# Kernel optimization log

Measured on AMD Instinct MI355X. Metric: run time of the kernel, lower is better.

The kernel has to match this reference:

```python
import jax, jax.numpy as jnp
import numpy as np
import math

DIM = 1536; NH = 12; HD = 128
F, H, W = 6, 30, 30
S = F * H * W
B = 1
K_LEN = 9900  # hardcoded k_lens in the source forward
EPS_NORM = 1e-6


def _rope_tables(max_len=1024, d=HD):
    # Wan rope_params: three tables of widths d-4*(d//6), 2*(d//6), 2*(d//6)
    # -> cos/sin tables of half-widths 22, 21, 21 (concat = d//2 = 64)
    def ang(dd):
        inv = 1.0 / (10000.0 ** (np.arange(0, dd, 2, dtype=np.float64) / dd))
        return np.outer(np.arange(max_len, dtype=np.float64), inv)
    a = np.concatenate([ang(d - 4 * (d // 6)), ang(2 * (d // 6)), ang(2 * (d // 6))], axis=1)
    return np.cos(a).astype(np.float32), np.sin(a).astype(np.float32)


def setup_inputs() -> dict:
    key = jax.random.key(0)
    ks = jax.random.split(key, 5)
    s = 1.0 / math.sqrt(DIM)
    cos, sin = _rope_tables()
    return {
        "x": jax.random.normal(ks[0], (B, S, DIM), jnp.float32),
        "q_w": jax.random.normal(ks[1], (DIM, DIM), jnp.float32) * s,
        "q_b": jnp.zeros((DIM,), jnp.float32),
        "k_w": jax.random.normal(ks[2], (DIM, DIM), jnp.float32) * s,
        "k_b": jnp.zeros((DIM,), jnp.float32),
        "v_w": jax.random.normal(ks[3], (DIM, DIM), jnp.float32) * s,
        "v_b": jnp.zeros((DIM,), jnp.float32),
        "o_w": jax.random.normal(ks[4], (DIM, DIM), jnp.float32) * s,
        "o_b": jnp.zeros((DIM,), jnp.float32),
        "norm_q_w": jnp.ones((DIM,), jnp.float32),
        "norm_k_w": jnp.ones((DIM,), jnp.float32),
        "freqs_cos": jnp.asarray(cos),
        "freqs_sin": jnp.asarray(sin),
        "grid_f": F, "grid_h": H, "grid_w": W,
    }


def rms_norm(x, w):
    # RMSNorm over full model dim, computed in fp32 (as in source)
    xf = x.astype(jnp.float32)
    xn = xf * jax.lax.rsqrt(jnp.mean(xf * xf, axis=-1, keepdims=True) + EPS_NORM)
    return xn.astype(x.dtype) * w


def rope_apply(x, cos, sin, f, h, w):
    # x: [B,S,N,D]; rotate consecutive pairs with 3D-factorized (f,h,w) freqs
    Bb, Ss, Nn, Dd = x.shape
    c = Dd // 2
    sp = [c - 2 * (c // 3), c // 3, c // 3]  # 22, 21, 21

    def grid(tab):
        tf = tab[:, :sp[0]]
        th = tab[:, sp[0]:sp[0] + sp[1]]
        tw = tab[:, sp[0] + sp[1]:]
        g = jnp.concatenate([
            jnp.broadcast_to(tf[:f, None, None, :], (f, h, w, sp[0])),
            jnp.broadcast_to(th[None, :h, None, :], (f, h, w, sp[1])),
            jnp.broadcast_to(tw[None, None, :w, :], (f, h, w, sp[2])),
        ], axis=-1)
        return g.reshape(f * h * w, 1, c)  # [S,1,c] (broadcast over heads)

    gc, gs = grid(cos), grid(sin)
    xp = x.astype(jnp.float32).reshape(Bb, Ss, Nn, c, 2)
    xr, xi = xp[..., 0], xp[..., 1]
    orr = xr * gc - xi * gs
    oii = xr * gs + xi * gc
    return jnp.stack([orr, oii], axis=-1).reshape(Bb, Ss, Nn, Dd).astype(x.dtype)


def attention(q, k, v, k_len):
    # full attention (window_size=(-1,-1)) with keys masked beyond k_len
    scale = 1.0 / math.sqrt(q.shape[-1])
    att = jnp.einsum('bqnd,bknd->bnqk', q, k) * scale
    valid = jnp.arange(k.shape[1]) < k_len
    att = jnp.where(valid[None, None, None, :], att, jnp.finfo(att.dtype).min)
    p = jax.nn.softmax(att, axis=-1)
    return jnp.einsum('bnqk,bknd->bqnd', p, v)


def reference(x, q_w, q_b, k_w, k_b, v_w, v_b, o_w, o_b, norm_q_w, norm_k_w, freqs_cos, freqs_sin, grid_f, grid_h, grid_w):
    Bb, Ss, _ = x.shape
    q = rms_norm(x @ q_w.T + q_b, norm_q_w).reshape(Bb, Ss, NH, HD)
    k = rms_norm(x @ k_w.T + k_b, norm_k_w).reshape(Bb, Ss, NH, HD)
    v = (x @ v_w.T + v_b).reshape(Bb, Ss, NH, HD)
    q = rope_apply(q, freqs_cos, freqs_sin, grid_f, grid_h, grid_w)
    k = rope_apply(k, freqs_cos, freqs_sin, grid_f, grid_h, grid_w)
    o = attention(q, k, v, K_LEN).reshape(Bb, Ss, NH * HD)
    return o @ o_w.T + o_b
```

## Files before the change

kernel.cpp:

```cpp
#include <hip/hip_runtime.h>

#define DIM 1536
#define NH 12
#define HD 128
#define S_LEN 5400
#define SPAD 5440
#define MPAD 5504
#define MPAD2 5632
#define NQKV 4608
#define EPS_NORM 1e-6f

typedef __bf16 bf16_t;
typedef __bf16 bf16x8 __attribute__((ext_vector_type(8)));
typedef __bf16 bf16x4 __attribute__((ext_vector_type(4)));
typedef __bf16 bf16x2 __attribute__((ext_vector_type(2)));
typedef float  f32x4  __attribute__((ext_vector_type(4)));
typedef float  f32x16 __attribute__((ext_vector_type(16)));
typedef int    i32x2  __attribute__((ext_vector_type(2)));

#define GLOAD_LDS16(gp, lp) __builtin_amdgcn_global_load_lds( \
    (__attribute__((address_space(1))) void*)(void*)(gp),     \
    (__attribute__((address_space(3))) void*)(lp), 16, 0, 0)

__device__ __forceinline__ unsigned int pkbf(float a, float b) {
  union { bf16x2 h; unsigned int u; } c;
  c.h[0] = (__bf16)a; c.h[1] = (__bf16)b;
  return c.u;
}

__device__ __forceinline__ float xhalf_max(float x) {
  i32x2 r = __builtin_amdgcn_permlane32_swap(__float_as_int(x), __float_as_int(x),
                                             false, false);
  return fmaxf(__int_as_float(r.x), __int_as_float(r.y));
}
__device__ __forceinline__ float xhalf_sum(float x) {
  i32x2 r = __builtin_amdgcn_permlane32_swap(__float_as_int(x), __float_as_int(x),
                                             false, false);
  return __int_as_float(r.x) + __int_as_float(r.y);
}


#define CVT_NX 8448
#define CVT_NW 6912
#define CVT_NO 2304

__global__ __launch_bounds__(256) void cvt_all_kernel(
    const float* __restrict__ x, const float* __restrict__ qw,
    const float* __restrict__ kw, const float* __restrict__ vw,
    const float* __restrict__ ow, bf16_t* __restrict__ xb,
    bf16_t* __restrict__ wqkv, bf16_t* __restrict__ wob) {
  int b = blockIdx.x;
  if (b < CVT_NX) {
    size_t base = ((size_t)b * 256 + threadIdx.x) * 4;
    size_t row = base / DIM;
    float4 v = make_float4(0.f, 0.f, 0.f, 0.f);
    if (row < S_LEN) v = *(const float4*)&x[base];
    bf16x4 o; o[0] = (__bf16)v.x; o[1] = (__bf16)v.y; o[2] = (__bf16)v.z; o[3] = (__bf16)v.w;
    *(bf16x4*)&xb[base] = o;
  } else if (b < CVT_NX + CVT_NW) {
    size_t base = ((size_t)(b - CVT_NX) * 256 + threadIdx.x) * 4;
    int row = (int)(base / DIM);
    int col = (int)(base - (size_t)row * DIM);
    const float* src; int rr = row;
    if (rr >= 3072)      { src = vw; rr -= 3072; }
    else if (rr >= 1536) { src = kw; rr -= 1536; }
    else                 { src = qw; }
    float4 v = *(const float4*)&src[(size_t)rr * DIM + col];
    bf16x4 o; o[0] = (__bf16)v.x; o[1] = (__bf16)v.y; o[2] = (__bf16)v.z; o[3] = (__bf16)v.w;
    *(bf16x4*)&wqkv[base] = o;
  } else {
    size_t base = ((size_t)(b - CVT_NX - CVT_NW) * 256 + threadIdx.x) * 4;
    float4 v = *(const float4*)&ow[base];
    bf16x4 o; o[0] = (__bf16)v.x; o[1] = (__bf16)v.y; o[2] = (__bf16)v.z; o[3] = (__bf16)v.w;
    *(bf16x4*)&wob[base] = o;
  }
}


__global__ __launch_bounds__(512, 2) void gemm1_256_kernel(
    const bf16_t* __restrict__ A, const bf16_t* __restrict__ B,
    bf16_t* __restrict__ C, bf16_t* __restrict__ vt,
    const float* __restrict__ bias0, const float* __restrict__ bias1,
    const float* __restrict__ bias2) {
  const int K = 1536, N = NQKV, KT = 24;
  __shared__ bf16_t lds[2][2][256 * 64];
  int tid = threadIdx.x;
  int lane = tid & 63, wave = tid >> 6, quad = lane >> 4, l16 = lane & 15;
  int wm2 = wave >> 2, wn4 = wave & 3;
  int m0 = blockIdx.y * 256, n0 = blockIdx.x * 256;
  const bf16_t* Ab = A + (size_t)m0 * K;
  const bf16_t* Bb = B + (size_t)n0 * K;
  f32x4 acc[8][4] = {};

  int srow = tid >> 3, spc = tid & 7;
  int ldst = srow * 64 + spc * 8;
  int sc8 = (spc ^ (srow & 7)) * 8;

#define G1_STAGE(buf, op, q, kt) \
  GLOAD_LDS16((op ? Bb : Ab) + (size_t)((q) * 64 + srow) * K + (kt) + sc8, \
              &lds[buf][op][(q) * 64 * 64 + ldst])

  G1_STAGE(0, 1, 0, 0); G1_STAGE(0, 1, 1, 0);
  G1_STAGE(0, 1, 2, 0); G1_STAGE(0, 1, 3, 0);
  G1_STAGE(0, 0, 0, 0); G1_STAGE(0, 0, 2, 0);
  G1_STAGE(0, 0, 1, 0); G1_STAGE(0, 0, 3, 0);

  int pcq0 = (0 * 4 + quad) ^ (l16 & 7);
  int pcq1 = (1 * 4 + quad) ^ (l16 & 7);

  for (int t = 0; t < KT; t++) {
    int cur = t & 1, nxt = cur ^ 1;
    int kn = (t + 1) * 64;
    bool st = (t + 1 < KT);

#define G1_PHASE(mh, nh2, STAGES, WAITS)                                      \
    {                                                                         \
      WAITS;                                                                  \
      __builtin_amdgcn_s_barrier();                                           \
      __builtin_amdgcn_sched_barrier(0);                                      \
      bf16x8 af[4][2], bfv[2][2];                                             \
      _Pragma("unroll")                                                       \
      for (int i2 = 0; i2 < 4; i2++) {                                        \
        int row = wm2 * 128 + ((mh) * 4 + i2) * 16 + l16;                     \
        af[i2][0] = *(const bf16x8*)&lds[cur][0][row * 64 + pcq0 * 8];        \
        af[i2][1] = *(const bf16x8*)&lds[cur][0][row * 64 + pcq1 * 8];        \
      }                                                                       \
      _Pragma("unroll")                                                       \
      for (int j2 = 0; j2 < 2; j2++) {                                        \
        int rowb = wn4 * 64 + ((nh2) * 2 + j2) * 16 + l16;                    \
        bfv[j2][0] = *(const bf16x8*)&lds[cur][1][rowb * 64 + pcq0 * 8];      \
        bfv[j2][1] = *(const bf16x8*)&lds[cur][1][rowb * 64 + pcq1 * 8];      \
      }                                                                       \
      if (st) { STAGES; }                                                     \
      asm volatile("s_waitcnt lgkmcnt(0)" ::: "memory");                      \
      __builtin_amdgcn_sched_barrier(0);                                      \
      __builtin_amdgcn_s_setprio(1);                                          \
      _Pragma("unroll")                                                       \
      for (int i2 = 0; i2 < 4; i2++)                                          \
        _Pragma("unroll")                                                     \
        for (int j2 = 0; j2 < 2; j2++)                                        \
          _Pragma("unroll")                                                   \
          for (int kk = 0; kk < 2; kk++)                                      \
            acc[(mh) * 4 + i2][(nh2) * 2 + j2] =                              \
                __builtin_amdgcn_mfma_f32_16x16x32_bf16(                      \
                    af[i2][kk], bfv[j2][kk],                                  \
                    acc[(mh) * 4 + i2][(nh2) * 2 + j2], 0, 0, 0);             \
      __builtin_amdgcn_s_setprio(0);                                          \
    }

    G1_PHASE(0, 0, G1_STAGE(nxt,1,0,kn); G1_STAGE(nxt,1,1,kn),
             if (st) asm volatile("s_waitcnt vmcnt(2)" ::: "memory");
             else    asm volatile("s_waitcnt vmcnt(0)" ::: "memory"));
    G1_PHASE(1, 0, G1_STAGE(nxt,1,2,kn); G1_STAGE(nxt,1,3,kn),
             if (st) asm volatile("s_waitcnt vmcnt(2)" ::: "memory");
             else    asm volatile("s_waitcnt vmcnt(0)" ::: "memory"));
    G1_PHASE(0, 1, G1_STAGE(nxt,0,0,kn); G1_STAGE(nxt,0,2,kn),
             asm volatile("s_waitcnt vmcnt(4)" ::: "memory"));
    G1_PHASE(1, 1, G1_STAGE(nxt,0,1,kn); G1_STAGE(nxt,0,3,kn),
             asm volatile("s_waitcnt vmcnt(6)" ::: "memory"));
#undef G1_PHASE
  }
#undef G1_STAGE

  bool isv = (n0 >= 3072);
#pragma unroll
  for (int j = 0; j < 4; j++) {
    int n = n0 + wn4 * 64 + j * 16 + l16;
    float bias = (n < 1536) ? bias0[n] : (n < 3072) ? bias1[n - 1536] : bias2[n - 3072];
    if (!isv) {
#pragma unroll
      for (int i = 0; i < 8; i++) {
#pragma unroll
        for (int r = 0; r < 4; r++) {
          int m = m0 + wm2 * 128 + i * 16 + quad * 4 + r;
          C[(size_t)m * N + n] = (__bf16)(acc[i][j][r] + bias);
        }
      }
    } else {
      int nd = n - 3072;
      bf16_t* vrow = vt + ((size_t)(nd >> 7) * HD + (nd & 127)) * SPAD;
#pragma unroll
      for (int i = 0; i < 8; i++) {
        int m = m0 + wm2 * 128 + i * 16 + quad * 4;
        if (m < SPAD) {
          bf16x4 vv;
#pragma unroll
          for (int r = 0; r < 4; r++) {
            float val = acc[i][j][r] + bias;
            vv[r] = (m + r < S_LEN) ? (__bf16)val : (__bf16)0.f;
          }
          *(bf16x4*)&vrow[m] = vv;
        }
      }
    }
  }
}


template<bool OUT_BF16>
__global__ __launch_bounds__(256) void gemm_bt_kernel(
    const bf16_t* __restrict__ A, const bf16_t* __restrict__ B, void* __restrict__ C,
    const float* __restrict__ bias0, const float* __restrict__ bias1,
    const float* __restrict__ bias2, int M, int N, int K, int Mvalid) {
  __shared__ bf16_t As[2][128 * 32];
  __shared__ bf16_t Bs[2][128 * 32];
  int tid = threadIdx.x;
  int lane = tid & 63, wave = tid >> 6, quad = lane >> 4, l16 = lane & 15;
  int m0 = blockIdx.y * 128, n0 = blockIdx.x * 128;
  int wm = (wave >> 1) * 64, wn = (wave & 1) * 64;
  const bf16_t* Ab = A + (size_t)m0 * K;
  const bf16_t* Bb = B + (size_t)n0 * K;
  f32x4 acc[4][4] = {};

  int eo0 = tid * 8;
  int row0 = eo0 >> 5, col0 = eo0 & 31;
  int eo1 = (256 + tid) * 8;
  int row1 = eo1 >> 5, col1 = eo1 & 31;

  GLOAD_LDS16(Ab + (size_t)row0 * K + col0, &As[0][eo0]);
  GLOAD_LDS16(Bb + (size_t)row0 * K + col0, &Bs[0][eo0]);
  GLOAD_LDS16(Ab + (size_t)row1 * K + col1, &As[0][eo1]);
  GLOAD_LDS16(Bb + (size_t)row1 * K + col1, &Bs[0][eo1]);
  asm volatile("s_waitcnt vmcnt(0)" ::: "memory");
  __builtin_amdgcn_s_barrier();
  __builtin_amdgcn_sched_barrier(0);

  int KT = K >> 5;
  for (int t = 0; t < KT; t++) {
    int cur = t & 1;
    if (t + 1 < KT) {
      int kn = (t + 1) << 5;
      GLOAD_LDS16(Ab + (size_t)row0 * K + kn + col0, &As[cur ^ 1][eo0]);
      GLOAD_LDS16(Bb + (size_t)row0 * K + kn + col0, &Bs[cur ^ 1][eo0]);
      GLOAD_LDS16(Ab + (size_t)row1 * K + kn + col1, &As[cur ^ 1][eo1]);
      GLOAD_LDS16(Bb + (size_t)row1 * K + kn + col1, &Bs[cur ^ 1][eo1]);
    }
    bf16x8 af[4], bfr[4];
#pragma unroll
    for (int i = 0; i < 4; i++)
      af[i] = *(const bf16x8*)&As[cur][(wm + i * 16 + l16) * 32 + quad * 8];
#pragma unroll
    for (int j = 0; j < 4; j++)
      bfr[j] = *(const bf16x8*)&Bs[cur][(wn + j * 16 + l16) * 32 + quad * 8];
#pragma unroll
    for (int i = 0; i < 4; i++)
#pragma unroll
      for (int j = 0; j < 4; j++)
        acc[i][j] = __builtin_amdgcn_mfma_f32_16x16x32_bf16(af[i], bfr[j], acc[i][j], 0, 0, 0);
    asm volatile("s_waitcnt vmcnt(0) lgkmcnt(0)" ::: "memory");
    __builtin_amdgcn_s_barrier();
    __builtin_amdgcn_sched_barrier(0);
  }
#pragma unroll
  for (int j = 0; j < 4; j++) {
    int n = n0 + wn + j * 16 + l16;
    float bias = (n < 1536) ? bias0[n] : (n < 3072) ? bias1[n - 1536] : bias2[n - 3072];
#pragma unroll
    for (int i = 0; i < 4; i++) {
#pragma unroll
      for (int r = 0; r < 4; r++) {
        int m = m0 + wm + i * 16 + quad * 4 + r;
        float v = acc[i][j][r] + bias;
        if (OUT_BF16) {
          ((bf16_t*)C)[(size_t)m * N + n] = (__bf16)v;
        } else {
          if (m < Mvalid) ((float*)C)[(size_t)m * N + n] = v;
        }
      }
    }
  }
}


__global__ __launch_bounds__(256) void rope_qk_kernel(
    const bf16_t* __restrict__ qkv, const float* __restrict__ nqw,
    const float* __restrict__ nkw, const float* __restrict__ fcos,
    const float* __restrict__ fsin, bf16_t* __restrict__ qout,
    bf16_t* __restrict__ kout) {
  int s = blockIdx.x;
  int tid = threadIdx.x;
  bool valid = s < S_LEN;
  int f = s / 900, hh = (s / 30) % 30, ww = s % 30;
  __shared__ float red[4];
  for (int which = 0; which < 2; which++) {
    const bf16_t* src = qkv + (size_t)s * NQKV + which * DIM;
    const float* nw = which ? nkw : nqw;
    bf16_t* dst = (which ? kout : qout) + (size_t)s * DIM;
    float osc = which ? 1.0f : 0.12751742686f;
    float v[6]; float ss = 0.f;
#pragma unroll
    for (int i = 0; i < 6; i++) {
      v[i] = valid ? (float)src[tid * 6 + i] : 0.f;
      ss += v[i] * v[i];
    }
#pragma unroll
    for (int off = 32; off >= 1; off >>= 1) ss += __shfl_down(ss, off);
    if ((tid & 63) == 0) red[tid >> 6] = ss;
    __syncthreads();
    float tot = red[0] + red[1] + red[2] + red[3];
    float rn = rsqrtf(tot * (1.f / DIM) + EPS_NORM);
    __syncthreads();
#pragma unroll
    for (int i = 0; i < 3; i++) {
      int e0 = tid * 6 + 2 * i;
      int p = e0 >> 1;
      int cc = p & 63;
      int pos = (cc < 22) ? f : (cc < 43) ? hh : ww;
      float c = fcos[pos * 64 + cc], sn = fsin[pos * 64 + cc];
      float xr = v[2 * i] * rn * nw[e0];
      float xi = v[2 * i + 1] * rn * nw[e0 + 1];
      dst[e0]     = (__bf16)((xr * c - xi * sn) * osc);
      dst[e0 + 1] = (__bf16)((xr * sn + xi * c) * osc);
    }
  }
}


__global__ __launch_bounds__(256, 2) void flash_attn_kernel(
    const bf16_t* __restrict__ q, const bf16_t* __restrict__ k,
    const bf16_t* __restrict__ vt, bf16_t* __restrict__ o) {
  __shared__ bf16_t Ks[2][64 * 128];
  __shared__ bf16_t Vs[2][64 * 128];
  int head = blockIdx.y;
  int s0 = blockIdx.x * 128;
  int tid = threadIdx.x, w = tid >> 6, lane = tid & 63;
  int l31 = lane & 31, hh = lane >> 5;

  bf16x8 bq[8];
  {
    const bf16_t* qp = &q[(size_t)(s0 + w * 32 + l31) * DIM + head * HD + hh * 8];
#pragma unroll
    for (int kc = 0; kc < 8; kc++) bq[kc] = *(const bf16x8*)(qp + kc * 16);
  }

  float m_i = -1e30f, l_i = 0.f;
  f32x16 oacc[4] = {};

  const int NT = SPAD / 64;

#pragma unroll
  for (int it = 0; it < 4; it++) {
    int slot = it * 256 + tid;
    int row = slot >> 4, pc = slot & 15;
    int c = pc ^ (row & 15);
    GLOAD_LDS16(k + (size_t)row * DIM + head * HD + c * 8, &Ks[0][slot * 8]);
  }
#pragma unroll
  for (int it = 0; it < 4; it++) {
    int slot = it * 256 + tid;
    int row = slot >> 4, pc = slot & 15;
    int cp = pc ^ (row & 15);
    int d = 2 * row + (cp >> 3);
    GLOAD_LDS16(vt + ((size_t)head * HD + d) * SPAD + (cp & 7) * 8, &Vs[0][slot * 8]);
  }
  asm volatile("s_waitcnt vmcnt(0)" ::: "memory");
  __builtin_amdgcn_s_barrier();
  __builtin_amdgcn_sched_barrier(0);

  for (int t = 0; t < NT; t++) {
    int kt = t * 64;
    int cur = t & 1;

    if (t + 1 < NT) {
      int kn = kt + 64;
#pragma unroll
      for (int it = 0; it < 4; it++) {
        int slot = it * 256 + tid;
        int row = slot >> 4, pc = slot & 15;
        int c = pc ^ (row & 15);
        GLOAD_LDS16(k + (size_t)(kn + row) * DIM + head * HD + c * 8, &Ks[cur ^ 1][slot * 8]);
      }
#pragma unroll
      for (int it = 0; it < 4; it++) {
        int slot = it * 256 + tid;
        int row = slot >> 4, pc = slot & 15;
        int cp = pc ^ (row & 15);
        int d = 2 * row + (cp >> 3);
        GLOAD_LDS16(vt + ((size_t)head * HD + d) * SPAD + kn + (cp & 7) * 8, &Vs[cur ^ 1][slot * 8]);
      }
    }

    f32x16 sacc[2] = {};
    __builtin_amdgcn_s_setprio(1);
#pragma unroll
    for (int ns = 0; ns < 2; ns++) {
      int row = ns * 32 + l31;
#pragma unroll
      for (int kc = 0; kc < 8; kc++) {
        int pc = (kc * 2 + hh) ^ (row & 15);
        bf16x8 ak = *(const bf16x8*)&Ks[cur][row * 128 + pc * 8];
        sacc[ns] = __builtin_amdgcn_mfma_f32_32x32x16_bf16(ak, bq[kc], sacc[ns], 0, 0, 0);
      }
    }
    __builtin_amdgcn_s_setprio(0);

    if (kt + 64 > S_LEN) {
#pragma unroll
      for (int ns = 0; ns < 2; ns++)
#pragma unroll
        for (int r = 0; r < 16; r++) {
          int kvg = kt + ns * 32 + (r & 3) + 8 * (r >> 2) + 4 * hh;
          if (kvg >= S_LEN) sacc[ns][r] = -1e30f;
        }
    }

    float mx;
    {
      float tm[8];
#pragma unroll
      for (int i = 0; i < 8; i++)
        tm[i] = fmaxf(fmaxf(sacc[0][i], sacc[0][i + 8]),
                      fmaxf(sacc[1][i], sacc[1][i + 8]));
#pragma unroll
      for (int i = 0; i < 4; i++) tm[i] = fmaxf(tm[i], tm[i + 4]);
      mx = fmaxf(fmaxf(tm[0], tm[2]), fmaxf(tm[1], tm[3]));
    }
    mx = xhalf_max(mx);
    if (!__all(mx - m_i <= 11.5f)) {
      float mn = fmaxf(m_i, mx);
      float al = __builtin_amdgcn_exp2f(m_i - mn);
      l_i *= al;
#pragma unroll
      for (int dt = 0; dt < 4; dt++)
#pragma unroll
        for (int r = 0; r < 16; r++) oacc[dt][r] *= al;
      m_i = mn;
    }
#pragma unroll
    for (int ns = 0; ns < 2; ns++)
#pragma unroll
      for (int r = 0; r < 16; r++)
        sacc[ns][r] = __builtin_amdgcn_exp2f(sacc[ns][r] - m_i);
    float rs;
    {
      float ts[8];
#pragma unroll
      for (int i = 0; i < 8; i++)
        ts[i] = (sacc[0][i] + sacc[0][i + 8]) + (sacc[1][i] + sacc[1][i + 8]);
#pragma unroll
      for (int i = 0; i < 4; i++) ts[i] += ts[i + 4];
      rs = (ts[0] + ts[2]) + (ts[1] + ts[3]);
    }
    l_i += xhalf_sum(rs);

    __builtin_amdgcn_s_setprio(1);
#pragma unroll
    for (int kvc = 0; kvc < 4; kvc++) {
      int ns = kvc >> 1, rb = (kvc & 1) * 8;
      int w0 = (int)pkbf(sacc[ns][rb + 0], sacc[ns][rb + 1]);
      int w1 = (int)pkbf(sacc[ns][rb + 2], sacc[ns][rb + 3]);
      int w2 = (int)pkbf(sacc[ns][rb + 4], sacc[ns][rb + 5]);
      int w3 = (int)pkbf(sacc[ns][rb + 6], sacc[ns][rb + 7]);
      i32x2 r02 = __builtin_amdgcn_permlane32_swap(w0, w2, false, false);
      i32x2 r13 = __builtin_amdgcn_permlane32_swap(w1, w3, false, false);
      union { unsigned int u[4]; bf16x8 v8; } bpu;
      bpu.u[0] = (unsigned int)r02.x; bpu.u[1] = (unsigned int)r13.x;
      bpu.u[2] = (unsigned int)r02.y; bpu.u[3] = (unsigned int)r13.y;
      bf16x8 bp = bpu.v8;
#pragma unroll
      for (int dt = 0; dt < 4; dt++) {
        int d = dt * 32 + l31;
        int r = d >> 1;
        int cp = ((d & 1) << 3) | (kvc * 2 + hh);
        int pc = cp ^ (r & 15);
        bf16x8 av = *(const bf16x8*)&Vs[cur][r * 128 + pc * 8];
        oacc[dt] = __builtin_amdgcn_mfma_f32_32x32x16_bf16(av, bp, oacc[dt], 0, 0, 0);
      }
    }
    __builtin_amdgcn_s_setprio(0);

    asm volatile("s_waitcnt vmcnt(0) lgkmcnt(0)" ::: "memory");
    __builtin_amdgcn_s_barrier();
    __builtin_amdgcn_sched_barrier(0);
  }

  bf16_t* scr = ((bf16_t*)Ks) + w * (32 * 64);
  float inv = 1.f / l_i;
  int qr = lane >> 1, seg = lane & 1;
  int srow = s0 + w * 32 + qr;
#pragma unroll
  for (int half = 0; half < 2; half++) {
#pragma unroll
    for (int dl = 0; dl < 2; dl++) {
      int dt = half * 2 + dl;
#pragma unroll
      for (int tt = 0; tt < 4; tt++) {
        bf16x4 v;
#pragma unroll
        for (int r4 = 0; r4 < 4; r4++) v[r4] = (__bf16)(oacc[dt][tt * 4 + r4] * inv);
        int c8 = dl * 8 + 2 * tt + hh;
        int pc8 = c8 ^ (l31 & 15);
        *(bf16x4*)&scr[l31 * 64 + pc8 * 4] = v;
      }
    }
#pragma unroll
    for (int i = 0; i < 4; i++) {
      int c8 = seg * 8 + 2 * i;
      bf16x4 lo = *(const bf16x4*)&scr[qr * 64 + ((c8) ^ (qr & 15)) * 4];
      bf16x4 hi = *(const bf16x4*)&scr[qr * 64 + ((c8 + 1) ^ (qr & 15)) * 4];
      bf16x8 val;
#pragma unroll
      for (int j = 0; j < 4; j++) { val[j] = lo[j]; val[j + 4] = hi[j]; }
      if (srow < S_LEN)
        *(bf16x8*)&o[(size_t)srow * DIM + head * HD + half * 64 + seg * 32 + i * 8] = val;
    }
  }
}


extern "C" void kernel_launch(void* const* d_in, const int* in_sizes, int n_in,
                              void* d_out, int out_size, void* d_ws, size_t ws_size,
                              hipStream_t stream) {
  const float* x    = (const float*)d_in[0];
  const float* q_w  = (const float*)d_in[1];
  const float* q_b  = (const float*)d_in[2];
  const float* k_w  = (const float*)d_in[3];
  const float* k_b  = (const float*)d_in[4];
  const float* v_w  = (const float*)d_in[5];
  const float* v_b  = (const float*)d_in[6];
  const float* o_w  = (const float*)d_in[7];
  const float* o_b  = (const float*)d_in[8];
  const float* nqw  = (const float*)d_in[9];
  const float* nkw  = (const float*)d_in[10];
  const float* fcos = (const float*)d_in[11];
  const float* fsin = (const float*)d_in[12];

  char* ws = (char*)d_ws;
  bf16_t* xb   = (bf16_t*)(ws + 0);
  bf16_t* wqkv = (bf16_t*)(ws + 17301504);
  bf16_t* wob  = (bf16_t*)(ws + 31457280);
  bf16_t* qkv  = (bf16_t*)(ws + 36175872);
  bf16_t* qb   = (bf16_t*)(ws + 88080384);
  bf16_t* kb   = (bf16_t*)(ws + 104988672);
  bf16_t* vtb  = (bf16_t*)(ws + 121896960);
  bf16_t* aob  = (bf16_t*)(ws + 36175872);

  cvt_all_kernel<<<CVT_NX + CVT_NW + CVT_NO, 256, 0, stream>>>(
      x, q_w, k_w, v_w, o_w, xb, wqkv, wob);

  gemm1_256_kernel<<<dim3(NQKV / 256, MPAD2 / 256), 512, 0, stream>>>(
      xb, wqkv, qkv, vtb, q_b, k_b, v_b);

  rope_qk_kernel<<<MPAD, 256, 0, stream>>>(qkv, nqw, nkw, fcos, fsin, qb, kb);

  flash_attn_kernel<<<dim3(MPAD / 128, NH), 256, 0, stream>>>(qb, kb, vtb, aob);

  gemm_bt_kernel<false><<<dim3(DIM / 128, MPAD / 128), 256, 0, stream>>>(
      aob, wob, d_out, o_b, o_b, o_b, MPAD, DIM, DIM, S_LEN);
}
```

Baseline: 631.1 us.

## Split KV tiles across two wave groups in flash attention and merge partials

```diff
diff --git a/kernel.cpp b/kernel.cpp
--- a/kernel.cpp
+++ b/kernel.cpp
@@ -316,19 +316,21 @@
 }
 
 
-__global__ __launch_bounds__(256, 2) void flash_attn_kernel(
+__global__ __launch_bounds__(512, 4) void flash_attn_kernel(
     const bf16_t* __restrict__ q, const bf16_t* __restrict__ k,
     const bf16_t* __restrict__ vt, bf16_t* __restrict__ o) {
   __shared__ bf16_t Ks[2][64 * 128];
   __shared__ bf16_t Vs[2][64 * 128];
+  __shared__ float ml1[4][2][32];
   int head = blockIdx.y;
   int s0 = blockIdx.x * 128;
   int tid = threadIdx.x, w = tid >> 6, lane = tid & 63;
+  int g = w & 3, st = w >> 2;
   int l31 = lane & 31, hh = lane >> 5;
 
   bf16x8 bq[8];
   {
-    const bf16_t* qp = &q[(size_t)(s0 + w * 32 + l31) * DIM + head * HD + hh * 8];
+    const bf16_t* qp = &q[(size_t)(s0 + g * 32 + l31) * DIM + head * HD + hh * 8];
 #pragma unroll
     for (int kc = 0; kc < 8; kc++) bq[kc] = *(const bf16x8*)(qp + kc * 16);
   }
@@ -336,49 +338,34 @@
   float m_i = -1e30f, l_i = 0.f;
   f32x16 oacc[4] = {};
 
-  const int NT = SPAD / 64;
-
-#pragma unroll
-  for (int it = 0; it < 4; it++) {
-    int slot = it * 256 + tid;
-    int row = slot >> 4, pc = slot & 15;
-    int c = pc ^ (row & 15);
-    GLOAD_LDS16(k + (size_t)row * DIM + head * HD + c * 8, &Ks[0][slot * 8]);
-  }
-#pragma unroll
-  for (int it = 0; it < 4; it++) {
-    int slot = it * 256 + tid;
-    int row = slot >> 4, pc = slot & 15;
-    int cp = pc ^ (row & 15);
-    int d = 2 * row + (cp >> 3);
-    GLOAD_LDS16(vt + ((size_t)head * HD + d) * SPAD + (cp & 7) * 8, &Vs[0][slot * 8]);
-  }
-  asm volatile("s_waitcnt vmcnt(0)" ::: "memory");
-  __builtin_amdgcn_s_barrier();
-  __builtin_amdgcn_sched_barrier(0);
-
-  for (int t = 0; t < NT; t++) {
-    int kt = t * 64;
-    int cur = t & 1;
-
-    if (t + 1 < NT) {
-      int kn = kt + 64;
-#pragma unroll
-      for (int it = 0; it < 4; it++) {
-        int slot = it * 256 + tid;
-        int row = slot >> 4, pc = slot & 15;
-        int c = pc ^ (row & 15);
-        GLOAD_LDS16(k + (size_t)(kn + row) * DIM + head * HD + c * 8, &Ks[cur ^ 1][slot * 8]);
-      }
-#pragma unroll
-      for (int it = 0; it < 4; it++) {
-        int slot = it * 256 + tid;
-        int row = slot >> 4, pc = slot & 15;
-        int cp = pc ^ (row & 15);
-        int d = 2 * row + (cp >> 3);
-        GLOAD_LDS16(vt + ((size_t)head * HD + d) * SPAD + kn + (cp & 7) * 8, &Vs[cur ^ 1][slot * 8]);
-      }
-    }
+  const int NR = 43;
+
+  for (int r = 0; r < NR; r++) {
+#pragma unroll
+    for (int it = 0; it < 4; it++) {
+      int slot = it * 512 + tid;
+      int b = slot >> 10, sI = slot & 1023;
+      int row = sI >> 4, pc = sI & 15;
+      int c = pc ^ (row & 15);
+      int ktb = (2 * r + b) * 64;
+      GLOAD_LDS16(k + (size_t)(ktb + row) * DIM + head * HD + c * 8, &Ks[b][sI * 8]);
+    }
+#pragma unroll
+    for (int it = 0; it < 4; it++) {
+      int slot = it * 512 + tid;
+      int b = slot >> 10, sI = slot & 1023;
+      int row = sI >> 4, pc = sI & 15;
+      int cp = pc ^ (row & 15);
+      int d = 2 * row + (cp >> 3);
+      int ktv = (2 * r + b) * 64;
+      if (ktv > SPAD - 64) ktv = SPAD - 64;
+      GLOAD_LDS16(vt + ((size_t)head * HD + d) * SPAD + ktv + (cp & 7) * 8, &Vs[b][sI * 8]);
+    }
+    asm volatile("s_waitcnt vmcnt(0)" ::: "memory");
+    __builtin_amdgcn_s_barrier();
+    __builtin_amdgcn_sched_barrier(0);
+
+    int kt = (2 * r + st) * 64;
 
     f32x16 sacc[2] = {};
     __builtin_amdgcn_s_setprio(1);
@@ -388,7 +375,7 @@
 #pragma unroll
       for (int kc = 0; kc < 8; kc++) {
         int pc = (kc * 2 + hh) ^ (row & 15);
-        bf16x8 ak = *(const bf16x8*)&Ks[cur][row * 128 + pc * 8];
+        bf16x8 ak = *(const bf16x8*)&Ks[st][row * 128 + pc * 8];
         sacc[ns] = __builtin_amdgcn_mfma_f32_32x32x16_bf16(ak, bq[kc], sacc[ns], 0, 0, 0);
       }
     }
@@ -398,9 +385,9 @@
 #pragma unroll
       for (int ns = 0; ns < 2; ns++)
 #pragma unroll
-        for (int r = 0; r < 16; r++) {
-          int kvg = kt + ns * 32 + (r & 3) + 8 * (r >> 2) + 4 * hh;
-          if (kvg >= S_LEN) sacc[ns][r] = -1e30f;
+        for (int r2 = 0; r2 < 16; r2++) {
+          int kvg = kt + ns * 32 + (r2 & 3) + 8 * (r2 >> 2) + 4 * hh;
+          if (kvg >= S_LEN) sacc[ns][r2] = -1e30f;
         }
     }
 
@@ -423,14 +410,14 @@
 #pragma unroll
       for (int dt = 0; dt < 4; dt++)
 #pragma unroll
-        for (int r = 0; r < 16; r++) oacc[dt][r] *= al;
+        for (int r2 = 0; r2 < 16; r2++) oacc[dt][r2] *= al;
       m_i = mn;
     }
 #pragma unroll
     for (int ns = 0; ns < 2; ns++)
 #pragma unroll
-      for (int r = 0; r < 16; r++)
-        sacc[ns][r] = __builtin_amdgcn_exp2f(sacc[ns][r] - m_i);
+      for (int r2 = 0; r2 < 16; r2++)
+        sacc[ns][r2] = __builtin_amdgcn_exp2f(sacc[ns][r2] - m_i);
     float rs;
     {
       float ts[8];
@@ -460,24 +447,57 @@
 #pragma unroll
       for (int dt = 0; dt < 4; dt++) {
         int d = dt * 32 + l31;
-        int r = d >> 1;
+        int rr2 = d >> 1;
         int cp = ((d & 1) << 3) | (kvc * 2 + hh);
-        int pc = cp ^ (r & 15);
-        bf16x8 av = *(const bf16x8*)&Vs[cur][r * 128 + pc * 8];
+        int pc = cp ^ (rr2 & 15);
+        bf16x8 av = *(const bf16x8*)&Vs[st][rr2 * 128 + pc * 8];
         oacc[dt] = __builtin_amdgcn_mfma_f32_32x32x16_bf16(av, bp, oacc[dt], 0, 0, 0);
       }
     }
     __builtin_amdgcn_s_setprio(0);
 
-    asm volatile("s_waitcnt vmcnt(0) lgkmcnt(0)" ::: "memory");
+    asm volatile("s_waitcnt lgkmcnt(0)" ::: "memory");
     __builtin_amdgcn_s_barrier();
     __builtin_amdgcn_sched_barrier(0);
   }
 
-  bf16_t* scr = ((bf16_t*)Ks) + w * (32 * 64);
+  float* Og = (float*)((g < 2 ? (char*)Ks : (char*)Vs) + (g & 1) * 16384);
+  if (st == 1) {
+#pragma unroll
+    for (int dt = 0; dt < 4; dt++)
+#pragma unroll
+      for (int q4 = 0; q4 < 4; q4++) {
+        f32x4 vv;
+#pragma unroll
+        for (int r4 = 0; r4 < 4; r4++) vv[r4] = oacc[dt][q4 * 4 + r4];
+        *(f32x4*)&Og[((dt * 4 + q4) * 64 + lane) * 4] = vv;
+      }
+    if (hh == 0) { ml1[g][0][l31] = m_i; ml1[g][1][l31] = l_i; }
+  }
+  __syncthreads();
+  if (st == 1) return;
+
+  {
+    float m1v = ml1[g][0][l31], l1v = ml1[g][1][l31];
+    float mm = fmaxf(m_i, m1v);
+    float a0 = __builtin_amdgcn_exp2f(m_i - mm);
+    float a1 = __builtin_amdgcn_exp2f(m1v - mm);
+    l_i = l_i * a0 + l1v * a1;
+#pragma unroll
+    for (int dt = 0; dt < 4; dt++)
+#pragma unroll
+      for (int q4 = 0; q4 < 4; q4++) {
+        f32x4 vv = *(const f32x4*)&Og[((dt * 4 + q4) * 64 + lane) * 4];
+#pragma unroll
+        for (int r4 = 0; r4 < 4; r4++)
+          oacc[dt][q4 * 4 + r4] = oacc[dt][q4 * 4 + r4] * a0 + vv[r4] * a1;
+      }
+  }
+
+  bf16_t* scr = (bf16_t*)Og;
   float inv = 1.f / l_i;
   int qr = lane >> 1, seg = lane & 1;
-  int srow = s0 + w * 32 + qr;
+  int srow = s0 + g * 32 + qr;
 #pragma unroll
   for (int half = 0; half < 2; half++) {
 #pragma unroll
@@ -543,7 +563,7 @@
 
   rope_qk_kernel<<<MPAD, 256, 0, stream>>>(qkv, nqw, nkw, fcos, fsin, qb, kb);
 
-  flash_attn_kernel<<<dim3(MPAD / 128, NH), 256, 0, stream>>>(qb, kb, vtb, aob);
+  flash_attn_kernel<<<dim3(MPAD / 128, NH), 512, 0, stream>>>(qb, kb, vtb, aob);
 
   gemm_bt_kernel<false><<<dim3(DIM / 128, MPAD / 128), 256, 0, stream>>>(
       aob, wob, d_out, o_b, o_b, o_b, MPAD, DIM, DIM, S_LEN);
```

Result: slower. 1.207 ms (+91.2%).
